# Performance work log

Measured on AMD Instinct MI355X. Metric: run time of the kernel, lower is better.

Reference implementation:

```python
import jax, jax.numpy as jnp
import numpy as np

LORA_SCALING = 1.0 / 4.0  # lora_alpha / lora_rank
NUM_HEADS = 16
HEAD_DIM = 64
ROPE_BASE = 20000.0


def rotate_half(x):
    x1, x2 = jnp.split(x, 2, axis=-1)
    return jnp.concatenate([-x2, x1], axis=-1)


def setup_inputs() -> dict:
    key = jax.random.key(0)
    ks = jax.random.split(key, 8)
    B, S, D = 8, 1024, 1024
    hidden_states = jax.random.normal(ks[0], (B, S, D), jnp.float32)
    attention_mask = jnp.zeros((B, 1, 1, S), jnp.float32)
    # real rotary tables (HF style: duplicated half-dim freqs)
    inv_freq = 1.0 / (ROPE_BASE ** (jnp.arange(0, HEAD_DIM, 2, dtype=jnp.float32) / HEAD_DIM))
    t = jnp.arange(S, dtype=jnp.float32)
    freqs = jnp.outer(t, inv_freq)                      # [S, hd/2]
    emb = jnp.concatenate([freqs, freqs], axis=-1)      # [S, hd]
    cos = jnp.broadcast_to(jnp.cos(emb)[None], (B, S, HEAD_DIM))
    sin = jnp.broadcast_to(jnp.sin(emb)[None], (B, S, HEAD_DIM))
    adapter_mask = jax.random.randint(ks[1], (B,), 0, 5, jnp.int32)
    Wqkv_weight = jax.random.normal(ks[2], (3 * D, D), jnp.float32) * 0.02
    Wqkv_bias = jax.random.normal(ks[3], (3 * D,), jnp.float32) * 0.02
    lora_A = jax.random.normal(ks[4], (5, 4, D), jnp.float32) * 0.02
    lora_B = jax.random.normal(ks[5], (5, 3 * D, 4), jnp.float32) * 0.02
    return dict(hidden_states=hidden_states, attention_mask=attention_mask,
                cos=cos, sin=sin, adapter_mask=adapter_mask,
                Wqkv_weight=Wqkv_weight, Wqkv_bias=Wqkv_bias,
                lora_A=lora_A, lora_B=lora_B)


def reference(hidden_states, attention_mask, cos, sin, adapter_mask,
              Wqkv_weight, Wqkv_bias, lora_A, lora_B):
    B, S, D = hidden_states.shape
    H, hd = NUM_HEADS, HEAD_DIM
    # fused QKV projection with per-task LoRA (gather adapters per batch row)
    base = jnp.einsum('bsd,od->bso', hidden_states, Wqkv_weight) + Wqkv_bias
    A_t = lora_A[adapter_mask]                    # [B, r, D]
    B_t = lora_B[adapter_mask]                    # [B, 3D, r]
    lo = jnp.einsum('bsd,brd->bsr', hidden_states, A_t)
    delta = jnp.einsum('bsr,bor->bso', lo, B_t) * LORA_SCALING
    qkv = (base + delta).reshape(B, S, 3, H, hd)
    q = qkv[:, :, 0].transpose(0, 2, 1, 3)        # [B,H,S,hd]
    k = qkv[:, :, 1].transpose(0, 2, 1, 3)
    v = qkv[:, :, 2].transpose(0, 2, 1, 3)
    # inline RoPE
    c = cos[:, None, :, :]
    s = sin[:, None, :, :]
    q = q * c + rotate_half(q) * s
    k = k * c + rotate_half(k) * s
    # eager SDPA
    scaling = hd ** -0.5
    scores = jnp.einsum('bhqd,bhkd->bhqk', q, k) * scaling + attention_mask
    attn = jax.nn.softmax(scores, axis=-1)
    out = jnp.einsum('bhqk,bhkd->bhqd', attn, v)
    return out.transpose(0, 2, 1, 3).reshape(B, S, H * hd)
```

## Files before the change

kernel.cpp:

```cpp
#include <hip/hip_runtime.h>
#include <hip/hip_bf16.h>
#include <stdint.h>

typedef __attribute__((ext_vector_type(8))) short short8;
typedef __attribute__((ext_vector_type(4))) float f32x4;
typedef unsigned short ushort_t;

#define MFMA16(a, b, c) __builtin_amdgcn_mfma_f32_16x16x32_bf16((a), (b), (c), 0, 0, 0)
#define EXP2F(x) __builtin_amdgcn_exp2f(x)
#define BAR() __builtin_amdgcn_s_barrier()
#define LGKM0() do { asm volatile("s_waitcnt lgkmcnt(0)" ::: "memory"); \
                     __builtin_amdgcn_sched_barrier(0); } while (0)


__device__ __forceinline__ float bf2f(unsigned short u) {
    union { unsigned int i; float f; } x; x.i = ((unsigned int)u) << 16; return x.f;
}
__device__ __forceinline__ unsigned short f2bf(float f) {
    union { float f; unsigned int i; } x; x.f = f;
    unsigned int i = x.i;
    i = i + 0x7FFFu + ((i >> 16) & 1u);
    return (unsigned short)(i >> 16);
}
__device__ __forceinline__ unsigned int pack2(float a, float b) {
    return (unsigned int)f2bf(a) | ((unsigned int)f2bf(b) << 16);
}
__device__ __forceinline__ void glds16(const void* gsrc, void* ldst) {
    __builtin_amdgcn_global_load_lds(
        (const __attribute__((address_space(1))) unsigned int*)gsrc,
        (__attribute__((address_space(3))) unsigned int*)ldst, 16, 0, 0);
}

__global__ __launch_bounds__(64) void prep_kernel(
    const float* __restrict__ hidden,
    const float* __restrict__ W,
    const float* __restrict__ loraA,
    const int* __restrict__ adapter_mask,
    ushort_t* __restrict__ Hb,
    ushort_t* __restrict__ Wb,
    float4* __restrict__ lo)
{
    int blk = blockIdx.x;
    int lane = threadIdx.x;
    if (blk < 8192) {
        int b = blk >> 10;
        int a = adapter_mask[b];
        const float* hp = hidden + (size_t)blk * 1024 + lane * 16;
        float hv[16];
        for (int j = 0; j < 16; ++j) hv[j] = hp[j];
        uint4 p0, p1;
        p0.x = pack2(hv[0], hv[1]);  p0.y = pack2(hv[2], hv[3]);
        p0.z = pack2(hv[4], hv[5]);  p0.w = pack2(hv[6], hv[7]);
        p1.x = pack2(hv[8], hv[9]);  p1.y = pack2(hv[10], hv[11]);
        p1.z = pack2(hv[12], hv[13]); p1.w = pack2(hv[14], hv[15]);
        uint4* hd = (uint4*)(Hb + (size_t)blk * 1024 + lane * 16);
        hd[0] = p0; hd[1] = p1;
        const float* Ap = loraA + (size_t)a * 4096 + lane * 16;
        float acc[4];
        for (int r = 0; r < 4; ++r) {
            const float* ap = Ap + r * 1024;
            float s = 0.f;
            for (int j = 0; j < 16; ++j) s += hv[j] * ap[j];
            acc[r] = s;
        }
        for (int off = 32; off > 0; off >>= 1)
            for (int r = 0; r < 4; ++r) acc[r] += __shfl_xor(acc[r], off);
        if (lane == 0) lo[blk] = make_float4(acc[0], acc[1], acc[2], acc[3]);
    } else {
        int row = blk - 8192;
        const float* wp = W + (size_t)row * 1024 + lane * 16;
        float wv[16];
        for (int j = 0; j < 16; ++j) wv[j] = wp[j];
        uint4 p0, p1;
        p0.x = pack2(wv[0], wv[1]);  p0.y = pack2(wv[2], wv[3]);
        p0.z = pack2(wv[4], wv[5]);  p0.w = pack2(wv[6], wv[7]);
        p1.x = pack2(wv[8], wv[9]);  p1.y = pack2(wv[10], wv[11]);
        p1.z = pack2(wv[12], wv[13]); p1.w = pack2(wv[14], wv[15]);
        uint4* wd = (uint4*)(Wb + (size_t)row * 1024 + lane * 16);
        wd[0] = p0; wd[1] = p1;
    }
}

__global__ __launch_bounds__(512, 2) void qkv_gemm_kernel(
    const ushort_t* __restrict__ Hb,
    const ushort_t* __restrict__ Wb,
    const float* __restrict__ bias,
    const float4* __restrict__ lo,
    const float* __restrict__ loraB,
    const int* __restrict__ adapter_mask,
    const float* __restrict__ cosp,
    const float* __restrict__ sinp,
    ushort_t* __restrict__ qw,
    ushort_t* __restrict__ kw,
    ushort_t* __restrict__ vt)
{
    __shared__ __align__(16) ushort_t As[2][16384];
    __shared__ __align__(16) ushort_t Bs[2][16384];
    int tid = threadIdx.x;
    int wave = tid >> 6, lane = tid & 63, quad = lane >> 4, l16 = lane & 15;
    int wm = wave >> 2, wn = wave & 3;

    int wg = (blockIdx.x & 7) * 48 + (blockIdx.x >> 3);
    int bx = wg % 12, by = wg / 12;
    int n0 = bx * 256;
    int m0 = by * 256;

    int r_ = tid >> 3, c_ = (tid & 7) ^ (r_ & 7);
    const ushort_t* pA0 = Hb + (size_t)(m0 +   0 + r_) * 1024 + c_ * 8;
    const ushort_t* pA1 = Hb + (size_t)(m0 +  64 + r_) * 1024 + c_ * 8;
    const ushort_t* pA2 = Hb + (size_t)(m0 + 128 + r_) * 1024 + c_ * 8;
    const ushort_t* pA3 = Hb + (size_t)(m0 + 192 + r_) * 1024 + c_ * 8;
    const ushort_t* pB0 = Wb + (size_t)(n0 +   0 + r_) * 1024 + c_ * 8;
    const ushort_t* pB1 = Wb + (size_t)(n0 +  64 + r_) * 1024 + c_ * 8;
    const ushort_t* pB2 = Wb + (size_t)(n0 + 128 + r_) * 1024 + c_ * 8;
    const ushort_t* pB3 = Wb + (size_t)(n0 + 192 + r_) * 1024 + c_ * 8;
    char* stA0 = (char*)&As[0][0] + wave * 1024;
    char* stB0 = (char*)&Bs[0][0] + wave * 1024;

    f32x4 acc[8][4];
#pragma unroll
    for (int i = 0; i < 8; ++i)
#pragma unroll
        for (int j = 0; j < 4; ++j) acc[i][j] = (f32x4)0.f;

    glds16(pB0, stB0);          glds16(pB1, stB0 + 8192);
    glds16(pB2, stB0 + 16384);  glds16(pB3, stB0 + 24576);
    glds16(pA0, stA0);          glds16(pA1, stA0 + 8192);
    glds16(pA2, stA0 + 16384);  glds16(pA3, stA0 + 24576);
    glds16(pB0 + 64, stB0 + 32768);          glds16(pB1 + 64, stB0 + 32768 + 8192);
    glds16(pB2 + 64, stB0 + 32768 + 16384);  glds16(pB3 + 64, stB0 + 32768 + 24576);

    short8 bfr[4][2];
    short8 af0[2], af1[2];

#define AREADS(p) do {                                                              \
        int rl0 = (p) * 32 + l16;                                                   \
        int rl1 = rl0 + 16;                                                         \
        int u0 = wm * 2 + (rl0 >> 6), u1 = wm * 2 + (rl1 >> 6);                     \
        int rr0 = rl0 & 63, rr1 = rl1 & 63;                                         \
        af0[0] = *(const short8*)(rdA + u0 * 8192 + (rr0 * 8 + ((quad    ) ^ (rr0 & 7))) * 16); \
        af0[1] = *(const short8*)(rdA + u0 * 8192 + (rr0 * 8 + ((quad + 4) ^ (rr0 & 7))) * 16); \
        af1[0] = *(const short8*)(rdA + u1 * 8192 + (rr1 * 8 + ((quad    ) ^ (rr1 & 7))) * 16); \
        af1[1] = *(const short8*)(rdA + u1 * 8192 + (rr1 * 8 + ((quad + 4) ^ (rr1 & 7))) * 16); \
    } while (0)

#define PMFMA(p) do {                                                    \
        __builtin_amdgcn_s_setprio(1);                                   \
        acc[2*(p)  ][0] = MFMA16(af0[0], bfr[0][0], acc[2*(p)  ][0]);    \
        acc[2*(p)  ][1] = MFMA16(af0[0], bfr[1][0], acc[2*(p)  ][1]);    \
        acc[2*(p)  ][2] = MFMA16(af0[0], bfr[2][0], acc[2*(p)  ][2]);    \
        acc[2*(p)  ][3] = MFMA16(af0[0], bfr[3][0], acc[2*(p)  ][3]);    \
        acc[2*(p)+1][0] = MFMA16(af1[0], bfr[0][0], acc[2*(p)+1][0]);    \
        acc[2*(p)+1][1] = MFMA16(af1[0], bfr[1][0], acc[2*(p)+1][1]);    \
        acc[2*(p)+1][2] = MFMA16(af1[0], bfr[2][0], acc[2*(p)+1][2]);    \
        acc[2*(p)+1][3] = MFMA16(af1[0], bfr[3][0], acc[2*(p)+1][3]);    \
        acc[2*(p)  ][0] = MFMA16(af0[1], bfr[0][1], acc[2*(p)  ][0]);    \
        acc[2*(p)  ][1] = MFMA16(af0[1], bfr[1][1], acc[2*(p)  ][1]);    \
        acc[2*(p)  ][2] = MFMA16(af0[1], bfr[2][1], acc[2*(p)  ][2]);    \
        acc[2*(p)  ][3] = MFMA16(af0[1], bfr[3][1], acc[2*(p)  ][3]);    \
        acc[2*(p)+1][0] = MFMA16(af1[1], bfr[0][1], acc[2*(p)+1][0]);    \
        acc[2*(p)+1][1] = MFMA16(af1[1], bfr[1][1], acc[2*(p)+1][1]);    \
        acc[2*(p)+1][2] = MFMA16(af1[1], bfr[2][1], acc[2*(p)+1][2]);    \
        acc[2*(p)+1][3] = MFMA16(af1[1], bfr[3][1], acc[2*(p)+1][3]);    \
        __builtin_amdgcn_s_setprio(0);                                   \
    } while (0)

#pragma unroll 2
    for (int t = 0; t < 16; ++t) {
        int cur = t & 1;
        const char* rdA = (const char*)&As[0][0] + cur * 32768;
        const char* rdB = (const char*)&Bs[0][0] + cur * 32768;
        char* sA = stA0 + (cur ^ 1) * 32768;
        char* sB = stB0 + cur * 32768;
        int kA = (t + 1) << 6;
        int kB = (t + 2) << 6;
        bool doA = (t < 15), doB = (t < 14);

        if (t < 15) { asm volatile("s_waitcnt vmcnt(4)" ::: "memory"); }
        else        { asm volatile("s_waitcnt vmcnt(0)" ::: "memory"); }
        BAR();
#pragma unroll
        for (int ni = 0; ni < 4; ++ni) {
            int rb = ni * 16 + l16;
            bfr[ni][0] = *(const short8*)(rdB + wn * 8192 + (rb * 8 + ((quad    ) ^ (rb & 7))) * 16);
            bfr[ni][1] = *(const short8*)(rdB + wn * 8192 + (rb * 8 + ((quad + 4) ^ (rb & 7))) * 16);
        }
        AREADS(0);
        if (doA) { glds16(pA0 + kA, sA); glds16(pA1 + kA, sA + 8192); }
        BAR();
        LGKM0();
        PMFMA(0);

        BAR();
        AREADS(1);
        if (doA) { glds16(pA2 + kA, sA + 16384); glds16(pA3 + kA, sA + 24576); }
        BAR();
        LGKM0();
        PMFMA(1);

        BAR();
        AREADS(2);
        if (doB) { glds16(pB0 + kB, sB); glds16(pB1 + kB, sB + 8192); }
        BAR();
        LGKM0();
        PMFMA(2);

        BAR();
        AREADS(3);
        if (doB) { glds16(pB2 + kB, sB + 16384); glds16(pB3 + kB, sB + 24576); }
        BAR();
        LGKM0();
        PMFMA(3);
    }
#undef AREADS
#undef PMFMA

    int t_qkv = n0 >> 10;
    int b = m0 >> 10;
    int a_idx = adapter_mask[b];
    float bi[4], bb[4][4];
    int cpos[4], chh[4];
#pragma unroll
    for (int ni = 0; ni < 4; ++ni) {
        int c = n0 + wn * 64 + ni * 16 + l16;
        bi[ni] = bias[c];
        const float* Bp = loraB + ((size_t)a_idx * 3072 + c) * 4;
        bb[ni][0] = Bp[0]; bb[ni][1] = Bp[1]; bb[ni][2] = Bp[2]; bb[ni][3] = Bp[3];
        cpos[ni] = c & 63; chh[ni] = (c >> 6) & 15;
    }
#pragma unroll
    for (int mi = 0; mi < 8; ++mi) {
        float vals[4][4];
        int mrow0 = m0 + wm * 128 + mi * 16 + quad * 4;
#pragma unroll
        for (int r = 0; r < 4; ++r) {
            float4 lov = lo[mrow0 + r];
#pragma unroll
            for (int ni = 0; ni < 4; ++ni)
                vals[r][ni] = acc[mi][ni][r] + bi[ni]
                      + 0.25f * (lov.x * bb[ni][0] + lov.y * bb[ni][1]
                               + lov.z * bb[ni][2] + lov.w * bb[ni][3]);
        }
        int s0 = mrow0 & 1023;
        if (t_qkv < 2) {
#pragma unroll
            for (int r = 0; r < 4; ++r) {
                int s = s0 + r;
                size_t cb = ((size_t)b * 1024 + s) * 64;
                float cA = cosp[cb + l16],      sA_ = sinp[cb + l16];
                float cB = cosp[cb + 16 + l16], sB_ = sinp[cb + 16 + l16];
                float w0 = vals[r][0] * cA - vals[r][2] * sA_;
                float w2 = vals[r][2] * cA + vals[r][0] * sA_;
                float w1 = vals[r][1] * cB - vals[r][3] * sB_;
                float w3 = vals[r][3] * cB + vals[r][1] * sB_;
                float v[4] = {w0, w1, w2, w3};
#pragma unroll
                for (int ni = 0; ni < 4; ++ni) {
                    size_t bh = (size_t)b * 16 + chh[ni];
                    ushort_t ob = f2bf(v[ni]);
                    if (t_qkv == 0) qw[(bh * 1024 + s) * 64 + cpos[ni]] = ob;
                    else            kw[(bh * 1024 + s) * 64 + cpos[ni]] = ob;
                }
            }
        } else {
#pragma unroll
            for (int ni = 0; ni < 4; ++ni) {
                uint2 pk;
                pk.x = pack2(vals[0][ni], vals[1][ni]);
                pk.y = pack2(vals[2][ni], vals[3][ni]);
                size_t bh = (size_t)b * 16 + chh[ni];
                *(uint2*)&vt[(bh * 64 + cpos[ni]) * 1024 + s0] = pk;
            }
        }
    }
}

__global__ __launch_bounds__(256) void attn_kernel(
    const ushort_t* __restrict__ qw,
    const ushort_t* __restrict__ kw,
    const ushort_t* __restrict__ vt,
    const float* __restrict__ mask,
    float* __restrict__ out)
{
    __shared__ __align__(16) ushort_t Kt[2][4096];
    __shared__ __align__(16) ushort_t Vt[2][4096];
    __shared__ __align__(16) ushort_t Ps[4][32][72];
    __shared__ float mlds[1024];
    const float KSCALE = 0.125f * 1.44269504f;
    int tid = threadIdx.x;
    int wave = tid >> 6, lane = tid & 63, quad = lane >> 4, l16 = lane & 15;
    int id = blockIdx.x;
    int qt = id >> 7;
    int bh = id & 127;
    int b = bh >> 4, h = bh & 15;
    size_t base = (size_t)bh * 65536;
    int q0 = qt * 128 + wave * 32;

    for (int i = tid; i < 1024; i += 256) mlds[i] = mask[b * 1024 + i] * 1.44269504f;

    const ushort_t* kbase = kw + base;
    const ushort_t* vbase = vt + base;

    int n0 = tid, n1 = tid + 256;
    int r0 = n0 >> 3, c0 = (n0 & 7) ^ (r0 & 7);
    int r1 = n1 >> 3, c1 = (n1 & 7) ^ (r1 & 7);
    char* kd0[2] = { (char*)&Kt[0][0] + wave * 1024, (char*)&Kt[1][0] + wave * 1024 };
    char* vd0[2] = { (char*)&Vt[0][0] + wave * 1024, (char*)&Vt[1][0] + wave * 1024 };

    short8 qf[2][2];
    for (int mt = 0; mt < 2; ++mt)
        for (int kt = 0; kt < 2; ++kt)
            qf[mt][kt] = *(const short8*)(qw + base + (size_t)(q0 + mt * 16 + l16) * 64 + kt * 32 + quad * 8);

    f32x4 oacc[2][4], sum_acc[2];
    for (int mt = 0; mt < 2; ++mt) {
        sum_acc[mt] = (f32x4)0.f;
        for (int nt = 0; nt < 4; ++nt) oacc[mt][nt] = (f32x4)0.f;
    }

    short8 ones;
    for (int j = 0; j < 8; ++j) ones[j] = (short)0x3F80;

    glds16(kbase + (size_t)r0 * 64 + c0 * 8, kd0[0]);
    glds16(kbase + (size_t)r1 * 64 + c1 * 8, kd0[0] + 4096);
    glds16(vbase + (size_t)r0 * 1024 + c0 * 8, vd0[0]);
    glds16(vbase + (size_t)r1 * 1024 + c1 * 8, vd0[0] + 4096);

    int koff[4][2], voff[4][2];
    for (int nt = 0; nt < 4; ++nt)
        for (int kt = 0; kt < 2; ++kt) {
            int rr = nt * 16 + l16;
            int cc = (kt * 4 + quad) ^ (rr & 7);
            koff[nt][kt] = (rr * 8 + cc) * 8;
            voff[nt][kt] = (rr * 8 + cc) * 8;
        }

    for (int it = 0; it < 16; ++it) {
        int cur = it & 1;
        int kt0 = it * 64;
        __syncthreads();
        if (it < 15) {
            int kn = kt0 + 64;
            int nxt = cur ^ 1;
            glds16(kbase + (size_t)(kn + r0) * 64 + c0 * 8, kd0[nxt]);
            glds16(kbase + (size_t)(kn + r1) * 64 + c1 * 8, kd0[nxt] + 4096);
            glds16(vbase + (size_t)r0 * 1024 + kn + c0 * 8, vd0[nxt]);
            glds16(vbase + (size_t)r1 * 1024 + kn + c1 * 8, vd0[nxt] + 4096);
        }
        short8 kf[4][2];
        for (int nt = 0; nt < 4; ++nt)
            for (int kt = 0; kt < 2; ++kt)
                kf[nt][kt] = *(const short8*)&Kt[cur][koff[nt][kt]];
        f32x4 sacc[2][4];
        for (int mt = 0; mt < 2; ++mt)
            for (int nt = 0; nt < 4; ++nt) {
                f32x4 z = (f32x4)0.f;
                z = MFMA16(qf[mt][0], kf[nt][0], z);
                z = MFMA16(qf[mt][1], kf[nt][1], z);
                sacc[mt][nt] = z;
            }
        float mv[4];
        for (int nt = 0; nt < 4; ++nt) mv[nt] = mlds[kt0 + nt * 16 + l16];
        for (int mt = 0; mt < 2; ++mt)
            for (int nt = 0; nt < 4; ++nt)
                for (int r = 0; r < 4; ++r) {
                    float p = EXP2F(sacc[mt][nt][r] * KSCALE + mv[nt]);
                    Ps[wave][mt * 16 + quad * 4 + r][nt * 16 + l16] = f2bf(p);
                }
        short8 pf[2][2];
        for (int mt = 0; mt < 2; ++mt)
            for (int kt = 0; kt < 2; ++kt)
                pf[mt][kt] = *(const short8*)&Ps[wave][mt * 16 + l16][kt * 32 + quad * 8];
        short8 vf[4][2];
        for (int nt = 0; nt < 4; ++nt)
            for (int kt = 0; kt < 2; ++kt)
                vf[nt][kt] = *(const short8*)&Vt[cur][voff[nt][kt]];
        for (int mt = 0; mt < 2; ++mt) {
            for (int nt = 0; nt < 4; ++nt) {
                oacc[mt][nt] = MFMA16(pf[mt][0], vf[nt][0], oacc[mt][nt]);
                oacc[mt][nt] = MFMA16(pf[mt][1], vf[nt][1], oacc[mt][nt]);
            }
            sum_acc[mt] = MFMA16(pf[mt][0], ones, sum_acc[mt]);
            sum_acc[mt] = MFMA16(pf[mt][1], ones, sum_acc[mt]);
        }
    }

    for (int mt = 0; mt < 2; ++mt) {
        for (int r = 0; r < 4; ++r) {
            float inv = 1.f / sum_acc[mt][r];
            int s = q0 + mt * 16 + quad * 4 + r;
            size_t ob = ((size_t)b * 1024 + s) * 1024 + h * 64;
            for (int nt = 0; nt < 4; ++nt)
                out[ob + nt * 16 + l16] = oacc[mt][nt][r] * inv;
        }
    }
}

extern "C" void kernel_launch(void* const* d_in, const int* in_sizes, int n_in,
                              void* d_out, int out_size, void* d_ws, size_t ws_size,
                              hipStream_t stream)
{
    const float* hidden = (const float*)d_in[0];
    const float* mask   = (const float*)d_in[1];
    const float* cosp   = (const float*)d_in[2];
    const float* sinp   = (const float*)d_in[3];
    const int* adapter_mask = (const int*)d_in[4];
    const float* W      = (const float*)d_in[5];
    const float* bias   = (const float*)d_in[6];
    const float* loraA  = (const float*)d_in[7];
    const float* loraB  = (const float*)d_in[8];
    float* out = (float*)d_out;

    char* ws = (char*)d_ws;
    float4* lo = (float4*)ws;
    ushort_t* qw = (ushort_t*)(ws + (1 << 20));
    ushort_t* kw = qw + (size_t)8 * 16 * 1024 * 64;
    ushort_t* vt = kw + (size_t)8 * 16 * 1024 * 64;

    ushort_t* Hb = (ushort_t*)d_out;
    ushort_t* Wb = Hb + (size_t)8192 * 1024;

    prep_kernel<<<11264, 64, 0, stream>>>(hidden, W, loraA, adapter_mask, Hb, Wb, lo);
    qkv_gemm_kernel<<<384, 512, 0, stream>>>(Hb, Wb, bias, lo, loraB, adapter_mask,
                                             cosp, sinp, qw, kw, vt);
    attn_kernel<<<1024, 256, 0, stream>>>(qw, kw, vt, mask, out);
}
```

Measured before the change: 253.8 us.

## Triple-buffer K/V tiles in attention kernel with two-deep prefetch

Moves the attention kernel's K/V shared-memory staging from double to triple buffering. Two tiles are now prefetched ahead, and a partial vmcnt wait replaces the full wait so one tile's global loads stay in flight while another is consumed. This aims to hide global-to-LDS latency better. The cost is more LDS per block (an extra 16KB), which may reduce occupancy.

```diff
diff --git a/kernel.cpp b/kernel.cpp
--- a/kernel.cpp
+++ b/kernel.cpp
@@ -282,8 +282,8 @@
     const float* __restrict__ mask,
     float* __restrict__ out)
 {
-    __shared__ __align__(16) ushort_t Kt[2][4096];
-    __shared__ __align__(16) ushort_t Vt[2][4096];
+    __shared__ __align__(16) ushort_t Kt[3][4096];
+    __shared__ __align__(16) ushort_t Vt[3][4096];
     __shared__ __align__(16) ushort_t Ps[4][32][72];
     __shared__ float mlds[1024];
     const float KSCALE = 0.125f * 1.44269504f;
@@ -304,8 +304,6 @@
     int n0 = tid, n1 = tid + 256;
     int r0 = n0 >> 3, c0 = (n0 & 7) ^ (r0 & 7);
     int r1 = n1 >> 3, c1 = (n1 & 7) ^ (r1 & 7);
-    char* kd0[2] = { (char*)&Kt[0][0] + wave * 1024, (char*)&Kt[1][0] + wave * 1024 };
-    char* vd0[2] = { (char*)&Vt[0][0] + wave * 1024, (char*)&Vt[1][0] + wave * 1024 };
 
     short8 qf[2][2];
     for (int mt = 0; mt < 2; ++mt)
@@ -321,10 +319,7 @@
     short8 ones;
     for (int j = 0; j < 8; ++j) ones[j] = (short)0x3F80;
 
-    glds16(kbase + (size_t)r0 * 64 + c0 * 8, kd0[0]);
-    glds16(kbase + (size_t)r1 * 64 + c1 * 8, kd0[0] + 4096);
-    glds16(vbase + (size_t)r0 * 1024 + c0 * 8, vd0[0]);
-    glds16(vbase + (size_t)r1 * 1024 + c1 * 8, vd0[0] + 4096);
+    __syncthreads();
 
     int koff[4][2], voff[4][2];
     for (int nt = 0; nt < 4; ++nt)
@@ -335,22 +330,44 @@
             voff[nt][kt] = (rr * 8 + cc) * 8;
         }
 
+    {
+        char* kd = (char*)&Kt[0][0] + wave * 1024;
+        char* vd = (char*)&Vt[0][0] + wave * 1024;
+        glds16(kbase + (size_t)r0 * 64 + c0 * 8, kd);
+        glds16(kbase + (size_t)r1 * 64 + c1 * 8, kd + 4096);
+        glds16(vbase + (size_t)r0 * 1024 + c0 * 8, vd);
+        glds16(vbase + (size_t)r1 * 1024 + c1 * 8, vd + 4096);
+        kd = (char*)&Kt[1][0] + wave * 1024;
+        vd = (char*)&Vt[1][0] + wave * 1024;
+        glds16(kbase + (size_t)(64 + r0) * 64 + c0 * 8, kd);
+        glds16(kbase + (size_t)(64 + r1) * 64 + c1 * 8, kd + 4096);
+        glds16(vbase + (size_t)r0 * 1024 + 64 + c0 * 8, vd);
+        glds16(vbase + (size_t)r1 * 1024 + 64 + c1 * 8, vd + 4096);
+    }
+
+    const ushort_t* kR  = &Kt[0][0];  const ushort_t* vR  = &Vt[0][0];
+    const ushort_t* kN1 = &Kt[1][0];  const ushort_t* vN1 = &Vt[1][0];
+    const ushort_t* kN2 = &Kt[2][0];  const ushort_t* vN2 = &Vt[2][0];
+
     for (int it = 0; it < 16; ++it) {
-        int cur = it & 1;
         int kt0 = it * 64;
-        __syncthreads();
-        if (it < 15) {
-            int kn = kt0 + 64;
-            int nxt = cur ^ 1;
-            glds16(kbase + (size_t)(kn + r0) * 64 + c0 * 8, kd0[nxt]);
-            glds16(kbase + (size_t)(kn + r1) * 64 + c1 * 8, kd0[nxt] + 4096);
-            glds16(vbase + (size_t)r0 * 1024 + kn + c0 * 8, vd0[nxt]);
-            glds16(vbase + (size_t)r1 * 1024 + kn + c1 * 8, vd0[nxt] + 4096);
+        if (it < 15) { asm volatile("s_waitcnt vmcnt(4)" ::: "memory"); }
+        else         { asm volatile("s_waitcnt vmcnt(0)" ::: "memory"); }
+        BAR();
+        __builtin_amdgcn_sched_barrier(0);
+        if (it < 14) {
+            int kn = kt0 + 128;
+            char* kd = (char*)kN2 + wave * 1024;
+            char* vd = (char*)vN2 + wave * 1024;
+            glds16(kbase + (size_t)(kn + r0) * 64 + c0 * 8, kd);
+            glds16(kbase + (size_t)(kn + r1) * 64 + c1 * 8, kd + 4096);
+            glds16(vbase + (size_t)r0 * 1024 + kn + c0 * 8, vd);
+            glds16(vbase + (size_t)r1 * 1024 + kn + c1 * 8, vd + 4096);
         }
         short8 kf[4][2];
         for (int nt = 0; nt < 4; ++nt)
             for (int kt = 0; kt < 2; ++kt)
-                kf[nt][kt] = *(const short8*)&Kt[cur][koff[nt][kt]];
+                kf[nt][kt] = *(const short8*)&kR[koff[nt][kt]];
         f32x4 sacc[2][4];
         for (int mt = 0; mt < 2; ++mt)
             for (int nt = 0; nt < 4; ++nt) {
@@ -374,7 +391,7 @@
         short8 vf[4][2];
         for (int nt = 0; nt < 4; ++nt)
             for (int kt = 0; kt < 2; ++kt)
-                vf[nt][kt] = *(const short8*)&Vt[cur][voff[nt][kt]];
+                vf[nt][kt] = *(const short8*)&vR[voff[nt][kt]];
         for (int mt = 0; mt < 2; ++mt) {
             for (int nt = 0; nt < 4; ++nt) {
                 oacc[mt][nt] = MFMA16(pf[mt][0], vf[nt][0], oacc[mt][nt]);
@@ -383,6 +400,8 @@
             sum_acc[mt] = MFMA16(pf[mt][0], ones, sum_acc[mt]);
             sum_acc[mt] = MFMA16(pf[mt][1], ones, sum_acc[mt]);
         }
+        const ushort_t* tk = kR; kR = kN1; kN1 = kN2; kN2 = tk;
+        const ushort_t* tv = vR; vR = vN1; vN1 = vN2; vN2 = tv;
     }
 
     for (int mt = 0; mt < 2; ++mt) {
```

Result: no change. 249.6 us (-1.6%).
